# Performance work log

Hardware: AMD Instinct MI355X
Metric: run time of the kernel (lower is better)

## Reference

```python
import jax, jax.numpy as jnp
import numpy as np

N_NODES = 10000
N_EDGES = 160000
NEG_SLOPE = 0.2


def setup_inputs() -> dict:
    key = jax.random.key(0)
    ks = jax.random.split(key, 24)

    def rn(k, shape, scale):
        return (jax.random.normal(k, shape, dtype=jnp.float32) * scale)

    inp = {
        "x": rn(ks[0], (N_NODES, 128), 1.0),
        "edge_index": jax.random.randint(ks[1], (2, N_EDGES), 0, N_NODES, dtype=jnp.int32),
        "edge_attr": rn(ks[2], (N_EDGES, 8), 1.0),
        # GATConv 1: 128 -> 64 (heads=1)
        "W1": rn(ks[3], (128, 64), 0.09), "as1": rn(ks[4], (64,), 0.1), "ad1": rn(ks[5], (64,), 0.1), "b1": rn(ks[6], (64,), 0.01),
        # GATConv 2: 64 -> 256
        "W2": rn(ks[7], (64, 256), 0.125), "as2": rn(ks[8], (256,), 0.06), "ad2": rn(ks[9], (256,), 0.06), "b2": rn(ks[10], (256,), 0.01),
        # GATConv 3: 256 -> 1024
        "W3": rn(ks[11], (256, 1024), 0.0625), "as3": rn(ks[12], (1024,), 0.03), "ad3": rn(ks[13], (1024,), 0.03), "b3": rn(ks[14], (1024,), 0.01),
        # Dense head
        "lw1": rn(ks[15], (1024, 512), 0.03), "lb1": rn(ks[16], (512,), 0.01),
        "lw2": rn(ks[17], (512, 10), 0.04), "lb2": rn(ks[18], (10,), 0.01),
    }
    return inp


def gat_layer(x, src, dst, W, a_s, a_d, b, n):
    """PyG GATConv, heads=1, concat=True, add_self_loops handled by caller via src/dst."""
    h = x @ W                                   # [N, F_out]
    e = jax.nn.leaky_relu((h @ a_s)[src] + (h @ a_d)[dst], NEG_SLOPE)  # [E']
    m = jax.ops.segment_max(e, dst, num_segments=n)
    ex = jnp.exp(e - m[dst])
    denom = jax.ops.segment_sum(ex, dst, num_segments=n)
    alpha = ex / denom[dst]                     # scatter-softmax over incoming edges
    out = jax.ops.segment_sum(alpha[:, None] * h[src], dst, num_segments=n)
    return out + b


def reference(x, edge_index, edge_attr, W1, as1, ad1, b1, W2, as2, ad2, b2,
              W3, as3, ad3, b3, lw1, lb1, lw2, lb2):
    # edge_attr is accepted but ignored (GATConv built without edge_dim)
    n = x.shape[0]
    loops = jnp.arange(n, dtype=edge_index.dtype)  # add_self_loops=True
    src = jnp.concatenate([edge_index[0], loops])
    dst = jnp.concatenate([edge_index[1], loops])

    h = jax.nn.relu(gat_layer(x, src, dst, W1, as1, ad1, b1, n))
    h = jax.nn.relu(gat_layer(h, src, dst, W2, as2, ad2, b2, n))
    h = jax.nn.relu(gat_layer(h, src, dst, W3, as3, ad3, b3, n))

    pooled = jnp.max(h, axis=0, keepdims=True)  # global_max_pool, batch=None -> [1, 1024]
    z = jax.nn.relu(pooled @ lw1 + lb1)
    z = z @ lw2 + lb2
    return jax.nn.log_softmax(z, axis=1)
```

## Files before the change

kernel.cpp:

```cpp
#include <hip/hip_runtime.h>
#include <hip/hip_bf16.h>
#include <math.h>

#define NEG_SLOPE 0.2f
typedef unsigned short u16;
typedef short bf16x8 __attribute__((ext_vector_type(8)));
typedef float f32x4 __attribute__((ext_vector_type(4)));

__device__ __forceinline__ float bfu2f(u16 u) { return __uint_as_float(((unsigned)u) << 16); }
__device__ __forceinline__ u16 f2bu(float v) { return __bfloat16_as_ushort(__float2bfloat16(v)); }

__device__ __forceinline__ void gload_lds16(const void* g, void* l) {
    __builtin_amdgcn_global_load_lds((const __attribute__((address_space(1))) void*)g,
                                     (__attribute__((address_space(3))) void*)l, 16, 0, 0);
}

__global__ void prep_kernel(int* deg, int* cursor, float* pooled, int N,
                            const float* __restrict__ x, u16* __restrict__ xb,
                            const float* __restrict__ W1, u16* __restrict__ Wt1,
                            const float* __restrict__ W2, u16* __restrict__ Wt2,
                            const float* __restrict__ W3, u16* __restrict__ Wt3,
                            const float* __restrict__ as2, const float* __restrict__ ad2,
                            const float* __restrict__ as3, const float* __restrict__ ad3,
                            float* __restrict__ ws2, float* __restrict__ wd2,
                            float* __restrict__ ws3, float* __restrict__ wd3,
                            int c0, int c1, int c2, int c3, int c4) {
    int bid = blockIdx.x, tid = threadIdx.x;
    if (bid < c0) {
        int i = bid * 256 + tid;
        if (i < N) { deg[i] = 0; cursor[i] = 0; }
        if (i < 1024) pooled[i] = 0.f;
    } else if (bid < c1) {
        int i = (bid - c0) * 256 + tid;
        if (i < N * 128) xb[i] = f2bu(x[i]);
    } else if (bid < c2) {
        int i = (bid - c1) * 256 + tid;
        int k = i % 128, f = i / 128;
        Wt1[i] = f2bu(W1[k * 64 + f]);
    } else if (bid < c3) {
        int i = (bid - c2) * 256 + tid;
        int k = i % 64, f = i / 64;
        Wt2[i] = f2bu(W2[k * 256 + f]);
    } else if (bid < c4) {
        int i = (bid - c3) * 256 + tid;
        int k = i % 256, f = i / 256;
        Wt3[i] = f2bu(W3[(size_t)k * 1024 + f]);
    } else {
        int wv = ((bid - c4) * 256 + tid) >> 6;
        int lane = tid & 63;
        const float *W, *va, *vd; float *os, *od; int F, row;
        if (wv < 64) { W = W2; va = as2; vd = ad2; F = 256; row = wv; os = ws2; od = wd2; }
        else if (wv < 320) { W = W3; va = as3; vd = ad3; F = 1024; row = wv - 64; os = ws3; od = wd3; }
        else return;
        const float* wr = W + (size_t)row * F;
        float ss = 0.f, dd = 0.f;
        for (int f = lane; f < F; f += 64) { float wvv = wr[f]; ss += wvv * va[f]; dd += wvv * vd[f]; }
        for (int off = 32; off; off >>= 1) { ss += __shfl_xor(ss, off); dd += __shfl_xor(dd, off); }
        if (lane == 0) { os[row] = ss; od[row] = dd; }
    }
}

__global__ void count_kernel(const int* __restrict__ edst, int E, int N, int* deg) {
    int i = blockIdx.x * blockDim.x + threadIdx.x;
    int total = E + N;
    if (i >= total) return;
    int dn = (i < E) ? edst[i] : (i - E);
    atomicAdd(&deg[dn], 1);
}

__global__ void scan_kernel(const int* __restrict__ deg, int N, int* __restrict__ offsets) {
    __shared__ int part[257];
    int tid = threadIdx.x;
    int chunk = (N + 255) / 256;
    int begin = tid * chunk;
    int fin = begin + chunk; if (fin > N) fin = N; if (begin > N) begin = N;
    int sum = 0;
    for (int i = begin; i < fin; ++i) sum += deg[i];
    part[tid] = sum;
    __syncthreads();
    if (tid == 0) {
        int acc = 0;
        for (int t = 0; t < 256; ++t) { int v = part[t]; part[t] = acc; acc += v; }
        part[256] = acc;
    }
    __syncthreads();
    int acc = part[tid];
    for (int i = begin; i < fin; ++i) { offsets[i] = acc; acc += deg[i]; }
    if (tid == 255) offsets[N] = part[256];
}

__global__ void scatter_kernel(const int* __restrict__ esrc, const int* __restrict__ edst,
                               int E, int N, const int* __restrict__ offsets,
                               int* cursor, int* __restrict__ srcg) {
    int i = blockIdx.x * blockDim.x + threadIdx.x;
    int total = E + N;
    if (i >= total) return;
    int sn, dn;
    if (i < E) { sn = esrc[i]; dn = edst[i]; } else { sn = i - E; dn = i - E; }
    int pos = atomicAdd(&cursor[dn], 1);
    srcg[offsets[dn] + pos] = sn;
}

template <int K, int MR, bool BIASRELU, bool SD_EPI>
__global__ __launch_bounds__(256) void mfma_gemm(const u16* __restrict__ A,
                                                 const u16* __restrict__ Wt,
                                                 u16* __restrict__ C,
                                                 const float* __restrict__ bias,
                                                 int M, int F,
                                                 const float* __restrict__ asv,
                                                 const float* __restrict__ adv,
                                                 float* __restrict__ s_out,
                                                 float* __restrict__ d_out) {
    constexpr int NK = K / 32;
    int tid = threadIdx.x;
    int w = tid >> 6, l = tid & 63;
    int l15 = l & 15, q = l >> 4;
    int bm = blockIdx.x * (64 * MR);
    int bn = blockIdx.y * 64;
    int r0 = bm + w * (16 * MR);

    const u16* aptr[MR];
    int row[MR];
#pragma unroll
    for (int mr = 0; mr < MR; ++mr) {
        int r = r0 + mr * 16 + l15;
        row[mr] = r;
        int ar = (r < M) ? r : (M - 1);
        aptr[mr] = A + (size_t)ar * K + 8 * q;
    }
    const u16* bptr[4];
#pragma unroll
    for (int nt = 0; nt < 4; ++nt)
        bptr[nt] = Wt + (size_t)(bn + nt * 16 + l15) * K + 8 * q;

    f32x4 acc[MR][4];
#pragma unroll
    for (int mr = 0; mr < MR; ++mr)
#pragma unroll
        for (int nt = 0; nt < 4; ++nt) acc[mr][nt] = (f32x4){0.f, 0.f, 0.f, 0.f};

    bf16x8 a_cur[MR], b_cur[4], a_nxt[MR], b_nxt[4];
#pragma unroll
    for (int mr = 0; mr < MR; ++mr) a_cur[mr] = *(const bf16x8*)(aptr[mr]);
#pragma unroll
    for (int nt = 0; nt < 4; ++nt) b_cur[nt] = *(const bf16x8*)(bptr[nt]);

#pragma unroll
    for (int kk = 0; kk < NK; ++kk) {
        if (kk + 1 < NK) {
            int koff = (kk + 1) * 32;
#pragma unroll
            for (int mr = 0; mr < MR; ++mr) a_nxt[mr] = *(const bf16x8*)(aptr[mr] + koff);
#pragma unroll
            for (int nt = 0; nt < 4; ++nt) b_nxt[nt] = *(const bf16x8*)(bptr[nt] + koff);
        }
#pragma unroll
        for (int mr = 0; mr < MR; ++mr)
#pragma unroll
            for (int nt = 0; nt < 4; ++nt)
                acc[mr][nt] = __builtin_amdgcn_mfma_f32_16x16x32_bf16(b_cur[nt], a_cur[mr], acc[mr][nt], 0, 0, 0);
        if (kk + 1 < NK) {
#pragma unroll
            for (int mr = 0; mr < MR; ++mr) a_cur[mr] = a_nxt[mr];
#pragma unroll
            for (int nt = 0; nt < 4; ++nt) b_cur[nt] = b_nxt[nt];
        }
    }

#pragma unroll
    for (int mr = 0; mr < MR; ++mr) {
        if (row[mr] >= M) continue;
#pragma unroll
        for (int nt = 0; nt < 4; ++nt) {
            int col = bn + nt * 16 + 4 * q;
            ushort4 st;
#pragma unroll
            for (int r = 0; r < 4; ++r) {
                float v = acc[mr][nt][r];
                if (BIASRELU) { v += bias[col + r]; v = fmaxf(v, 0.f); }
                ((u16*)&st)[r] = f2bu(v);
            }
            *(ushort4*)(C + (size_t)row[mr] * F + col) = st;
        }
    }

    if constexpr (SD_EPI) {
        float ss = 0.f, dd = 0.f;
#pragma unroll
        for (int nt = 0; nt < 4; ++nt)
#pragma unroll
            for (int r = 0; r < 4; ++r) {
                int col = nt * 16 + 4 * q + r;
                float v = acc[0][nt][r];
                ss += v * asv[col];
                dd += v * adv[col];
            }
        ss += __shfl_xor(ss, 16); ss += __shfl_xor(ss, 32);
        dd += __shfl_xor(dd, 16); dd += __shfl_xor(dd, 32);
        if (q == 0 && row[0] < M) { s_out[row[0]] = ss; d_out[row[0]] = dd; }
    }
}

__global__ __launch_bounds__(512) void gemm3_kernel(const u16* __restrict__ A,
                                                    const u16* __restrict__ Wt,
                                                    const float* __restrict__ bias,
                                                    int M,
                                                    float* __restrict__ pmaxbuf) {
    constexpr int K = 256;
    constexpr int ABYTES = 128 * 512;
    __shared__ char lds[2 * ABYTES];
    int tid = threadIdx.x;
    int w = tid >> 6, lane = tid & 63;
    int w2 = w >> 2, wc = w & 3;
    int l15 = lane & 15, q = lane >> 4;
    int bid = blockIdx.x;
    int rb = bid >> 2, cbp = bid & 3;
    int bm = rb * 128;

#pragma unroll
    for (int it = 0; it < 8; ++it) {
        int c = it * 512 + tid;
        int row = c >> 5, kc = c & 31;
        int arow = bm + row; if (arow >= M) arow = M - 1;
        gload_lds16(A + (size_t)arow * K + ((kc ^ (row & 7)) * 8),
                    lds + (size_t)(it * 512 + (tid & ~63)) * 16);
    }

    const char* abase = lds;
    char* bldst = lds + ABYTES;

    for (int half = 0; half < 2; ++half) {
        if (half) __syncthreads();
        int bn = cbp * 256 + half * 128;
#pragma unroll
        for (int it = 0; it < 8; ++it) {
            int c = it * 512 + tid;
            int col = c >> 5, kc = c & 31;
            gload_lds16(Wt + (size_t)(bn + col) * K + ((kc ^ (col & 7)) * 8),
                        bldst + (size_t)(it * 512 + (tid & ~63)) * 16);
        }
        __syncthreads();

        f32x4 acc[4][2];
#pragma unroll
        for (int mr = 0; mr < 4; ++mr)
#pragma unroll
            for (int nt = 0; nt < 2; ++nt) acc[mr][nt] = (f32x4){0.f, 0.f, 0.f, 0.f};

        const char* bbase = bldst;
#pragma unroll
        for (int kk = 0; kk < 8; ++kk) {
            int c = kk * 4 + q;
            bf16x8 af[4], bfr[2];
#pragma unroll
            for (int mr = 0; mr < 4; ++mr) {
                int row = w2 * 64 + mr * 16 + l15;
                af[mr] = *(const bf16x8*)(abase + row * 512 + ((c ^ (row & 7)) * 16));
            }
#pragma unroll
            for (int nt = 0; nt < 2; ++nt) {
                int col = wc * 32 + nt * 16 + l15;
                bfr[nt] = *(const bf16x8*)(bbase + col * 512 + ((c ^ (col & 7)) * 16));
            }
#pragma unroll
            for (int mr = 0; mr < 4; ++mr)
#pragma unroll
                for (int nt = 0; nt < 2; ++nt)
                    acc[mr][nt] = __builtin_amdgcn_mfma_f32_16x16x32_bf16(bfr[nt], af[mr], acc[mr][nt], 0, 0, 0);
        }

        float pmax[2][4];
#pragma unroll
        for (int nt = 0; nt < 2; ++nt)
#pragma unroll
            for (int r = 0; r < 4; ++r) pmax[nt][r] = 0.f;
#pragma unroll
        for (int mr = 0; mr < 4; ++mr) {
            bool valid = (bm + w2 * 64 + mr * 16 + l15) < M;
#pragma unroll
            for (int nt = 0; nt < 2; ++nt)
#pragma unroll
                for (int r = 0; r < 4; ++r) {
                    float v = acc[mr][nt][r] + bias[bn + wc * 32 + nt * 16 + 4 * q + r];
                    v = fmaxf(v, 0.f);
                    if (valid) pmax[nt][r] = fmaxf(pmax[nt][r], v);
                }
        }
#pragma unroll
        for (int nt = 0; nt < 2; ++nt)
#pragma unroll
            for (int r = 0; r < 4; ++r) {
#pragma unroll
                for (int msk = 1; msk < 16; msk <<= 1)
                    pmax[nt][r] = fmaxf(pmax[nt][r], __shfl_xor(pmax[nt][r], msk));
            }
        if (l15 == 0) {
#pragma unroll
            for (int nt = 0; nt < 2; ++nt)
#pragma unroll
                for (int r = 0; r < 4; ++r)
                    pmaxbuf[(size_t)(rb * 2 + w2) * 1024 + bn + wc * 32 + nt * 16 + 4 * q + r] = pmax[nt][r];
        }
    }
}

__global__ void sd_kernel(const u16* __restrict__ h, const float* __restrict__ a_s,
                          const float* __restrict__ a_d, int N, int F,
                          float* __restrict__ s, float* __restrict__ d) {
    int wave = (blockIdx.x * blockDim.x + threadIdx.x) >> 6;
    int lane = threadIdx.x & 63;
    if (wave >= N) return;
    const u16* hrow = h + (size_t)wave * F;
    float ss = 0.f, dd = 0.f;
    for (int f = lane * 4; f < F; f += 256) {
        ushort4 u = *reinterpret_cast<const ushort4*>(hrow + f);
        float4 av = *reinterpret_cast<const float4*>(a_s + f);
        float4 dv = *reinterpret_cast<const float4*>(a_d + f);
        float h0 = bfu2f(u.x), h1 = bfu2f(u.y), h2 = bfu2f(u.z), h3 = bfu2f(u.w);
        ss += h0 * av.x + h1 * av.y + h2 * av.z + h3 * av.w;
        dd += h0 * dv.x + h1 * dv.y + h2 * dv.z + h3 * dv.w;
    }
    for (int off = 32; off; off >>= 1) { ss += __shfl_xor(ss, off); dd += __shfl_xor(dd, off); }
    if (lane == 0) { s[wave] = ss; d[wave] = dd; }
}

__global__ void alpha_kernel(const float* __restrict__ sv, const float* __restrict__ dvec,
                             const int* __restrict__ srcg, const int* __restrict__ offsets,
                             int N, float* __restrict__ ag) {
    int n = (blockIdx.x * blockDim.x + threadIdx.x) >> 6;
    int lane = threadIdx.x & 63;
    if (n >= N) return;
    int start = offsets[n], end = offsets[n + 1];
    float dval = dvec[n];
    if (end - start <= 64) {
        int j0 = start + lane;
        float e0 = -INFINITY;
        if (j0 < end) {
            float v = sv[srcg[j0]] + dval;
            e0 = (v >= 0.f) ? v : NEG_SLOPE * v;
        }
        float m = e0;
#pragma unroll
        for (int off = 32; off; off >>= 1) m = fmaxf(m, __shfl_xor(m, off));
        float p = (j0 < end) ? expf(e0 - m) : 0.f;
        float ls = p;
#pragma unroll
        for (int off = 32; off; off >>= 1) ls += __shfl_xor(ls, off);
        if (j0 < end) ag[j0] = p / ls;
    } else {
        float lmax = -INFINITY;
        for (int j = start + lane; j < end; j += 64) {
            float v = sv[srcg[j]] + dval; v = (v >= 0.f) ? v : NEG_SLOPE * v;
            lmax = fmaxf(lmax, v);
        }
#pragma unroll
        for (int off = 32; off; off >>= 1) lmax = fmaxf(lmax, __shfl_xor(lmax, off));
        float ls = 0.f;
        for (int j = start + lane; j < end; j += 64) {
            float v = sv[srcg[j]] + dval; v = (v >= 0.f) ? v : NEG_SLOPE * v;
            ls += expf(v - lmax);
        }
#pragma unroll
        for (int off = 32; off; off >>= 1) ls += __shfl_xor(ls, off);
        float inv = 1.f / ls;
        for (int j = start + lane; j < end; j += 64) {
            float v = sv[srcg[j]] + dval; v = (v >= 0.f) ? v : NEG_SLOPE * v;
            ag[j] = expf(v - lmax) * inv;
        }
    }
}

template <int F, int FS>
__global__ __launch_bounds__(256) void gather_kernel(const u16* __restrict__ h,
                                                     const float* __restrict__ ag,
                                                     const int* __restrict__ srcg,
                                                     const int* __restrict__ offsets,
                                                     u16* __restrict__ out) {
    constexpr int FB = F / FS;
    constexpr int VPT = FB / 64;
    __shared__ float aL[256];
    __shared__ int sL[256];
    __shared__ float red[3][FB];
    int n = blockIdx.x;
    int f0 = blockIdx.y * FB;
    int tid = threadIdx.x, w = tid >> 6, lane = tid & 63;
    int start = offsets[n], end = offsets[n + 1];
    int deg = end - start;
    float acc0 = 0.f, acc1 = 0.f;

    for (int base = 0; base < deg; base += 256) {
        int cnt = deg - base; if (cnt > 256) cnt = 256;
        if (base) __syncthreads();
        if (tid < cnt) { aL[tid] = ag[start + base + tid]; sL[tid] = srcg[start + base + tid]; }
        __syncthreads();
        int j = w;
        for (; j + 12 < cnt; j += 16) {
            float a0 = aL[j], a1 = aL[j + 4], a2 = aL[j + 8], a3 = aL[j + 12];
            const u16* p0 = h + (size_t)sL[j] * F + f0 + lane * VPT;
            const u16* p1 = h + (size_t)sL[j + 4] * F + f0 + lane * VPT;
            const u16* p2 = h + (size_t)sL[j + 8] * F + f0 + lane * VPT;
            const u16* p3 = h + (size_t)sL[j + 12] * F + f0 + lane * VPT;
            ushort2 u0 = *(const ushort2*)p0;
            ushort2 u1 = *(const ushort2*)p1;
            ushort2 u2 = *(const ushort2*)p2;
            ushort2 u3 = *(const ushort2*)p3;
            acc0 += a0 * bfu2f(u0.x) + a1 * bfu2f(u1.x) + a2 * bfu2f(u2.x) + a3 * bfu2f(u3.x);
            acc1 += a0 * bfu2f(u0.y) + a1 * bfu2f(u1.y) + a2 * bfu2f(u2.y) + a3 * bfu2f(u3.y);
        }
        for (; j < cnt; j += 4) {
            float a = aL[j];
            ushort2 u = *(const ushort2*)(h + (size_t)sL[j] * F + f0 + lane * VPT);
            acc0 += a * bfu2f(u.x);
            acc1 += a * bfu2f(u.y);
        }
    }

    if (w > 0) { red[w - 1][lane * 2] = acc0; red[w - 1][lane * 2 + 1] = acc1; }
    __syncthreads();
    if (w != 0) return;
    ushort2 st;
    float x0 = acc0 + red[0][lane * 2] + red[1][lane * 2] + red[2][lane * 2];
    float x1 = acc1 + red[0][lane * 2 + 1] + red[1][lane * 2 + 1] + red[2][lane * 2 + 1];
    st.x = f2bu(x0); st.y = f2bu(x1);
    *(ushort2*)(out + (size_t)n * F + f0 + lane * 2) = st;
}

template <int F, bool BIASRELU, bool SD_EPI>
__global__ __launch_bounds__(256) void agg_kernel(const u16* __restrict__ h,
                                                  const float* __restrict__ sv,
                                                  const float* __restrict__ dvec,
                                                  const int* __restrict__ srcg,
                                                  const int* __restrict__ offsets,
                                                  const float* __restrict__ bias,
                                                  u16* __restrict__ out,
                                                  const float* __restrict__ wsv,
                                                  const float* __restrict__ wdv,
                                                  float* __restrict__ s_out,
                                                  float* __restrict__ d_out) {
    constexpr int VPT = F / 64;
    __shared__ float pL[256];
    __shared__ int sL[256];
    __shared__ float red[3][F];
    int n = blockIdx.x;
    int tid = threadIdx.x;
    int w = tid >> 6, lane = tid & 63;
    int start = offsets[n], end = offsets[n + 1];
    int deg = end - start;
    float dval = dvec[n];
    float acc[VPT];
#pragma unroll
    for (int v = 0; v < VPT; ++v) acc[v] = 0.f;
    float inv;

    auto gpoint = [&](int sn) { return h + (size_t)sn * F + lane * VPT; };
    auto accum = [&](float pw, const u16* hp) {
        if constexpr (VPT == 1) {
            acc[0] += pw * bfu2f(*hp);
        } else {
            ushort2 u = *(const ushort2*)hp;
            acc[0] += pw * bfu2f(u.x); acc[1] += pw * bfu2f(u.y);
        }
    };

    if (deg <= 256) {
        float e = -INFINITY;
        if (tid < deg) {
            int sn = srcg[start + tid];
            sL[tid] = sn;
            float v = sv[sn] + dval;
            e = (v >= 0.f) ? v : NEG_SLOPE * v;
        }
        pL[tid] = e;
        __syncthreads();
        float m = fmaxf(fmaxf(pL[lane], pL[lane + 64]), fmaxf(pL[lane + 128], pL[lane + 192]));
#pragma unroll
        for (int off2 = 32; off2; off2 >>= 1) m = fmaxf(m, __shfl_xor(m, off2));
        __syncthreads();
        float p = (tid < deg) ? expf(e - m) : 0.f;
        pL[tid] = p;
        __syncthreads();
        float t4 = (pL[lane] + pL[lane + 64]) + (pL[lane + 128] + pL[lane + 192]);
#pragma unroll
        for (int off2 = 32; off2; off2 >>= 1) t4 += __shfl_xor(t4, off2);
        inv = 1.f / t4;
        int jj = w;
        for (; jj + 12 < deg; jj += 16) {
            float p0 = pL[jj], p1 = pL[jj + 4], p2 = pL[jj + 8], p3 = pL[jj + 12];
            const u16* h0 = gpoint(sL[jj]);
            const u16* h1 = gpoint(sL[jj + 4]);
            const u16* h2 = gpoint(sL[jj + 8]);
            const u16* h3 = gpoint(sL[jj + 12]);
            accum(p0, h0); accum(p1, h1); accum(p2, h2); accum(p3, h3);
        }
        for (; jj < deg; jj += 4) accum(pL[jj], gpoint(sL[jj]));
    } else {
        float lmax = -INFINITY;
        for (int j = start + lane; j < end; j += 64) {
            float v = sv[srcg[j]] + dval; v = (v >= 0.f) ? v : NEG_SLOPE * v;
            lmax = fmaxf(lmax, v);
        }
#pragma unroll
        for (int off2 = 32; off2; off2 >>= 1) lmax = fmaxf(lmax, __shfl_xor(lmax, off2));
        float ls = 0.f;
        for (int j = start + lane; j < end; j += 64) {
            float v = sv[srcg[j]] + dval; v = (v >= 0.f) ? v : NEG_SLOPE * v;
            ls += expf(v - lmax);
        }
#pragma unroll
        for (int off2 = 32; off2; off2 >>= 1) ls += __shfl_xor(ls, off2);
        inv = 1.f / ls;
        for (int j = start + w; j < end; j += 4) {
            int sn = srcg[j];
            float e2 = sv[sn] + dval; e2 = (e2 >= 0.f) ? e2 : NEG_SLOPE * e2;
            accum(expf(e2 - lmax), gpoint(sn));
        }
    }

    if (w > 0) {
#pragma unroll
        for (int v = 0; v < VPT; ++v) red[w - 1][lane * VPT + v] = acc[v];
    }
    __syncthreads();
    if (w != 0) return;
    float res0 = 0.f;
    if constexpr (VPT == 1) {
        float xv = (acc[0] + red[0][lane] + red[1][lane] + red[2][lane]) * inv;
        if (BIASRELU) { xv += bias[lane]; xv = fmaxf(xv, 0.f); }
        res0 = xv;
        out[(size_t)n * F + lane] = f2bu(xv);
    } else {
        ushort2 st;
#pragma unroll
        for (int v = 0; v < VPT; ++v) {
            float xv = (acc[v] + red[0][lane * 2 + v] + red[1][lane * 2 + v] + red[2][lane * 2 + v]) * inv;
            if (BIASRELU) { xv += bias[lane * 2 + v]; xv = fmaxf(xv, 0.f); }
            ((u16*)&st)[v] = f2bu(xv);
        }
        *(ushort2*)(out + (size_t)n * F + lane * 2) = st;
    }
    if constexpr (SD_EPI) {
        float ss = res0 * wsv[lane], dd = res0 * wdv[lane];
        for (int off2 = 32; off2; off2 >>= 1) { ss += __shfl_xor(ss, off2); dd += __shfl_xor(dd, off2); }
        if (lane == 0) { s_out[n] = ss; d_out[n] = dd; }
    }
}

__global__ void head1ap_kernel(const float* __restrict__ pmaxbuf, int nslices,
                               const float* __restrict__ lw1, float* __restrict__ part) {
    __shared__ float pk[64];
    int tid = threadIdx.x;
    int k0 = blockIdx.y * 64;
    if (tid < 64) {
        float m = 0.f;
#pragma unroll 4
        for (int s = 0; s < nslices; ++s) m = fmaxf(m, pmaxbuf[(size_t)s * 1024 + k0 + tid]);
        pk[tid] = m;
    }
    __syncthreads();
    int j = blockIdx.x * 128 + tid;
    float acc = 0.f;
#pragma unroll 8
    for (int kk = 0; kk < 64; ++kk) acc += pk[kk] * lw1[(size_t)(k0 + kk) * 512 + j];
    part[blockIdx.y * 512 + j] = acc;
}

__global__ void head1bc_kernel(const float* __restrict__ part, const float* __restrict__ lb1,
                               const float* __restrict__ lw2, const float* __restrict__ lb2,
                               float* __restrict__ out) {
    __shared__ float zs[512];
    __shared__ float z2s[10];
    int tid = threadIdx.x;
    if (tid < 512) {
        float acc = lb1[tid];
#pragma unroll
        for (int t = 0; t < 16; ++t) acc += part[t * 512 + tid];
        zs[tid] = fmaxf(acc, 0.f);
    }
    __syncthreads();
    int w = tid >> 6, lane = tid & 63;
    if (w < 10) {
        float acc = 0.f;
#pragma unroll
        for (int kc = 0; kc < 8; ++kc) {
            int k = kc * 64 + lane;
            acc += zs[k] * lw2[k * 10 + w];
        }
        for (int off = 32; off; off >>= 1) acc += __shfl_xor(acc, off);
        if (lane == 0) z2s[w] = acc + lb2[w];
    }
    __syncthreads();
    if (tid == 0) {
        float m = z2s[0];
        for (int j = 1; j < 10; ++j) m = fmaxf(m, z2s[j]);
        float ssum = 0.f;
        for (int j = 0; j < 10; ++j) ssum += expf(z2s[j] - m);
        float lse = m + logf(ssum);
        for (int j = 0; j < 10; ++j) out[j] = z2s[j] - lse;
    }
}

extern "C" void kernel_launch(void* const* d_in, const int* in_sizes, int n_in,
                              void* d_out, int out_size, void* d_ws, size_t ws_size,
                              hipStream_t stream) {
    const float* x   = (const float*)d_in[0];
    const int* ei    = (const int*)d_in[1];
    const float* W1  = (const float*)d_in[3];
    const float* as1 = (const float*)d_in[4];
    const float* ad1 = (const float*)d_in[5];
    const float* b1  = (const float*)d_in[6];
    const float* W2  = (const float*)d_in[7];
    const float* as2 = (const float*)d_in[8];
    const float* ad2 = (const float*)d_in[9];
    const float* b2  = (const float*)d_in[10];
    const float* W3  = (const float*)d_in[11];
    const float* as3 = (const float*)d_in[12];
    const float* ad3 = (const float*)d_in[13];
    const float* b3  = (const float*)d_in[14];
    const float* lw1 = (const float*)d_in[15];
    const float* lb1 = (const float*)d_in[16];
    const float* lw2 = (const float*)d_in[17];
    const float* lb2 = (const float*)d_in[18];
    float* out = (float*)d_out;

    const int N = in_sizes[0] / 128;
    const int E = in_sizes[1] / 2;
    const int total = E + N;
    const int* esrc = ei;
    const int* edst = ei + E;

    char* base = (char*)d_ws;
    size_t off = 0;
    auto alloc = [&](size_t bytes) { void* p = base + off; off = (off + bytes + 255) & ~(size_t)255; return p; };
    u16* xb    = (u16*)alloc((size_t)N * 128 * 2);
    u16* h1    = (u16*)alloc((size_t)N * 64 * 2);
    u16* a1    = (u16*)alloc((size_t)N * 64 * 2);
    u16* agg2b = (u16*)alloc((size_t)N * 64 * 2);
    u16* a2    = (u16*)alloc((size_t)N * 256 * 2);
    u16* agg3b = (u16*)alloc((size_t)N * 256 * 2);
    u16* Wt1   = (u16*)alloc(128 * 64 * 2);
    u16* Wt2   = (u16*)alloc(64 * 256 * 2);
    u16* Wt3   = (u16*)alloc(256 * 1024 * 2);
    float* ws2 = (float*)alloc(64 * 4);
    float* wd2 = (float*)alloc(64 * 4);
    float* ws3 = (float*)alloc(256 * 4);
    float* wd3 = (float*)alloc(256 * 4);
    float* sbuf = (float*)alloc((size_t)N * 4);
    float* dbuf = (float*)alloc((size_t)N * 4);
    float* ag   = (float*)alloc((size_t)total * 4);
    float* pooled = (float*)alloc(1024 * 4);
    float* hpart  = (float*)alloc(16 * 512 * 4);
    int* deg     = (int*)alloc((size_t)N * 4);
    int* cursor  = (int*)alloc((size_t)N * 4);
    int* offsets = (int*)alloc((size_t)(N + 1) * 4);
    int* srcg    = (int*)alloc((size_t)total * 4);
    int nrb128g = (N + 127) / 128;
    float* pmaxbuf = (float*)alloc((size_t)nrb128g * 2 * 1024 * 4);

    const int TPB = 256;
    int gE = (total + TPB - 1) / TPB;
    int gW = (N + 3) / 4;
    int gR64 = (N + 63) / 64;
    int gR128 = (N + 127) / 128;

    int c0 = (N + 255) / 256;
    int c1 = c0 + (N * 128 + 255) / 256;
    int c2 = c1 + (128 * 64) / 256;
    int c3 = c2 + (64 * 256) / 256;
    int c4 = c3 + (256 * 1024) / 256;
    int gP = c4 + 80;
    prep_kernel<<<gP, TPB, 0, stream>>>(deg, cursor, pooled, N, x, xb,
                                        W1, Wt1, W2, Wt2, W3, Wt3,
                                        as2, ad2, as3, ad3, ws2, wd2, ws3, wd3,
                                        c0, c1, c2, c3, c4);

    count_kernel<<<gE, TPB, 0, stream>>>(edst, E, N, deg);
    scan_kernel<<<1, TPB, 0, stream>>>(deg, N, offsets);
    scatter_kernel<<<gE, TPB, 0, stream>>>(esrc, edst, E, N, offsets, cursor, srcg);

    mfma_gemm<128, 1, false, true><<<dim3(gR64, 1), TPB, 0, stream>>>(
        xb, Wt1, h1, nullptr, N, 64, as1, ad1, sbuf, dbuf);
    agg_kernel<64, true, true><<<N, TPB, 0, stream>>>(
        h1, sbuf, dbuf, srcg, offsets, b1, a1, ws2, wd2, sbuf, dbuf);

    agg_kernel<64, false, false><<<N, TPB, 0, stream>>>(
        a1, sbuf, dbuf, srcg, offsets, nullptr, agg2b, nullptr, nullptr, nullptr, nullptr);
    mfma_gemm<64, 2, true, false><<<dim3(gR128, 4), TPB, 0, stream>>>(
        agg2b, Wt2, a2, b2, N, 256, nullptr, nullptr, nullptr, nullptr);

    sd_kernel<<<gW, TPB, 0, stream>>>(a2, ws3, wd3, N, 256, sbuf, dbuf);
    alpha_kernel<<<gW, TPB, 0, stream>>>(sbuf, dbuf, srcg, offsets, N, ag);
    gather_kernel<256, 2><<<dim3(N, 2), TPB, 0, stream>>>(a2, ag, srcg, offsets, agg3b);
    gemm3_kernel<<<nrb128g * 4, 512, 0, stream>>>(agg3b, Wt3, b3, N, pmaxbuf);

    head1ap_kernel<<<dim3(4, 16), 128, 0, stream>>>(pmaxbuf, nrb128g * 2, lw1, hpart);
    head1bc_kernel<<<1, 640, 0, stream>>>(hpart, lb1, lw2, lb2, out);
}
```

Measured before the change: 190.1 us.

## Fuse x bf16 conversion into layer-1 GEMM, tile weight transposes, unroll gathers

The separate fp32-to-bf16 conversion of x in the prep kernel is dropped. A new gemm1 kernel instead reads fp32 x directly, converts it in registers, and double-buffers its loads. Weight transposes now go through 64x64 LDS tiles so both reads and writes are coalesced, and the unused pooled buffer init is removed. The gather loops in the aggregation kernels are unrolled from 4 to 8 neighbours per iteration to keep more loads in flight, at some cost in register pressure.

Measured after the change: 199.0 us. +4.6%, slower.

```diff
diff --git a/kernel.cpp b/kernel.cpp
--- a/kernel.cpp
+++ b/kernel.cpp
@@ -15,8 +15,7 @@
                                      (__attribute__((address_space(3))) void*)l, 16, 0, 0);
 }
 
-__global__ void prep_kernel(int* deg, int* cursor, float* pooled, int N,
-                            const float* __restrict__ x, u16* __restrict__ xb,
+__global__ void prep_kernel(int* deg, int* cursor, int N,
                             const float* __restrict__ W1, u16* __restrict__ Wt1,
                             const float* __restrict__ W2, u16* __restrict__ Wt2,
                             const float* __restrict__ W3, u16* __restrict__ Wt3,
@@ -24,29 +23,32 @@
                             const float* __restrict__ as3, const float* __restrict__ ad3,
                             float* __restrict__ ws2, float* __restrict__ wd2,
                             float* __restrict__ ws3, float* __restrict__ wd3,
-                            int c0, int c1, int c2, int c3, int c4) {
+                            int c0) {
+    __shared__ u16 sm[64][66];
     int bid = blockIdx.x, tid = threadIdx.x;
     if (bid < c0) {
         int i = bid * 256 + tid;
         if (i < N) { deg[i] = 0; cursor[i] = 0; }
-        if (i < 1024) pooled[i] = 0.f;
-    } else if (bid < c1) {
-        int i = (bid - c0) * 256 + tid;
-        if (i < N * 128) xb[i] = f2bu(x[i]);
-    } else if (bid < c2) {
-        int i = (bid - c1) * 256 + tid;
-        int k = i % 128, f = i / 128;
-        Wt1[i] = f2bu(W1[k * 64 + f]);
-    } else if (bid < c3) {
-        int i = (bid - c2) * 256 + tid;
-        int k = i % 64, f = i / 64;
-        Wt2[i] = f2bu(W2[k * 256 + f]);
-    } else if (bid < c4) {
-        int i = (bid - c3) * 256 + tid;
-        int k = i % 256, f = i / 256;
-        Wt3[i] = f2bu(W3[(size_t)k * 1024 + f]);
+    } else if (bid < c0 + 70) {
+        int tb = bid - c0;
+        const float* W; u16* Wt; int K, F, kt, ft;
+        if (tb < 2)      { W = W1; Wt = Wt1; K = 128; F = 64;   kt = tb;          ft = 0; }
+        else if (tb < 6) { W = W2; Wt = Wt2; K = 64;  F = 256;  kt = 0;           ft = tb - 2; }
+        else             { W = W3; Wt = Wt3; K = 256; F = 1024; kt = (tb - 6) & 3; ft = (tb - 6) >> 2; }
+        int ty = tid >> 6, tx = tid & 63;
+#pragma unroll
+        for (int r = 0; r < 16; ++r) {
+            int kl = r * 4 + ty;
+            sm[kl][tx] = f2bu(W[(size_t)(kt * 64 + kl) * F + ft * 64 + tx]);
+        }
+        __syncthreads();
+#pragma unroll
+        for (int r = 0; r < 16; ++r) {
+            int fl = r * 4 + ty;
+            Wt[(size_t)(ft * 64 + fl) * K + kt * 64 + tx] = sm[tx][fl];
+        }
     } else {
-        int wv = ((bid - c4) * 256 + tid) >> 6;
+        int wv = ((bid - c0 - 70) * 256 + tid) >> 6;
         int lane = tid & 63;
         const float *W, *va, *vd; float *os, *od; int F, row;
         if (wv < 64) { W = W2; va = as2; vd = ad2; F = 256; row = wv; os = ws2; od = wd2; }
@@ -101,16 +103,92 @@
     srcg[offsets[dn] + pos] = sn;
 }
 
-template <int K, int MR, bool BIASRELU, bool SD_EPI>
+__global__ __launch_bounds__(256) void gemm1_kernel(const float* __restrict__ X,
+                                                    const u16* __restrict__ Wt,
+                                                    u16* __restrict__ C,
+                                                    int M,
+                                                    const float* __restrict__ asv,
+                                                    const float* __restrict__ adv,
+                                                    float* __restrict__ s_out,
+                                                    float* __restrict__ d_out) {
+    constexpr int K = 128, NK = 4;
+    int tid = threadIdx.x;
+    int w = tid >> 6, l = tid & 63;
+    int l15 = l & 15, q = l >> 4;
+    int bm = blockIdx.x * 64;
+    int row = bm + w * 16 + l15;
+    int arow = (row < M) ? row : (M - 1);
+    const float* aptr = X + (size_t)arow * K + 8 * q;
+    const u16* bptr[4];
+#pragma unroll
+    for (int nt = 0; nt < 4; ++nt)
+        bptr[nt] = Wt + (size_t)(nt * 16 + l15) * K + 8 * q;
+
+    f32x4 acc[4];
+#pragma unroll
+    for (int nt = 0; nt < 4; ++nt) acc[nt] = (f32x4){0.f, 0.f, 0.f, 0.f};
+
+    float4 a0_cur = *(const float4*)(aptr);
+    float4 a1_cur = *(const float4*)(aptr + 4);
+    bf16x8 b_cur[4], b_nxt[4];
+    float4 a0_nxt, a1_nxt;
+#pragma unroll
+    for (int nt = 0; nt < 4; ++nt) b_cur[nt] = *(const bf16x8*)(bptr[nt]);
+
+#pragma unroll
+    for (int kk = 0; kk < NK; ++kk) {
+        if (kk + 1 < NK) {
+            int koff = (kk + 1) * 32;
+            a0_nxt = *(const float4*)(aptr + koff);
+            a1_nxt = *(const float4*)(aptr + koff + 4);
+#pragma unroll
+            for (int nt = 0; nt < 4; ++nt) b_nxt[nt] = *(const bf16x8*)(bptr[nt] + koff);
+        }
+        bf16x8 a8;
+        u16* ap = (u16*)&a8;
+        ap[0] = f2bu(a0_cur.x); ap[1] = f2bu(a0_cur.y); ap[2] = f2bu(a0_cur.z); ap[3] = f2bu(a0_cur.w);
+        ap[4] = f2bu(a1_cur.x); ap[5] = f2bu(a1_cur.y); ap[6] = f2bu(a1_cur.z); ap[7] = f2bu(a1_cur.w);
+#pragma unroll
+        for (int nt = 0; nt < 4; ++nt)
+            acc[nt] = __builtin_amdgcn_mfma_f32_16x16x32_bf16(b_cur[nt], a8, acc[nt], 0, 0, 0);
+        if (kk + 1 < NK) {
+            a0_cur = a0_nxt; a1_cur = a1_nxt;
+#pragma unroll
+            for (int nt = 0; nt < 4; ++nt) b_cur[nt] = b_nxt[nt];
+        }
+    }
+
+    if (row < M) {
+#pragma unroll
+        for (int nt = 0; nt < 4; ++nt) {
+            int col = nt * 16 + 4 * q;
+            ushort4 st;
+#pragma unroll
+            for (int r = 0; r < 4; ++r) ((u16*)&st)[r] = f2bu(acc[nt][r]);
+            *(ushort4*)(C + (size_t)row * 64 + col) = st;
+        }
+    }
+    float ss = 0.f, dd = 0.f;
+#pragma unroll
+    for (int nt = 0; nt < 4; ++nt)
+#pragma unroll
+        for (int r = 0; r < 4; ++r) {
+            int col = nt * 16 + 4 * q + r;
+            float v = acc[nt][r];
+            ss += v * asv[col];
+            dd += v * adv[col];
+        }
+    ss += __shfl_xor(ss, 16); ss += __shfl_xor(ss, 32);
+    dd += __shfl_xor(dd, 16); dd += __shfl_xor(dd, 32);
+    if (q == 0 && row < M) { s_out[row] = ss; d_out[row] = dd; }
+}
+
+template <int K, int MR, bool BIASRELU>
 __global__ __launch_bounds__(256) void mfma_gemm(const u16* __restrict__ A,
                                                  const u16* __restrict__ Wt,
                                                  u16* __restrict__ C,
                                                  const float* __restrict__ bias,
-                                                 int M, int F,
-                                                 const float* __restrict__ asv,
-                                                 const float* __restrict__ adv,
-                                                 float* __restrict__ s_out,
-                                                 float* __restrict__ d_out) {
+                                                 int M, int F) {
     constexpr int NK = K / 32;
     int tid = threadIdx.x;
     int w = tid >> 6, l = tid & 63;
@@ -182,22 +260,6 @@
             }
             *(ushort4*)(C + (size_t)row[mr] * F + col) = st;
         }
-    }
-
-    if constexpr (SD_EPI) {
-        float ss = 0.f, dd = 0.f;
-#pragma unroll
-        for (int nt = 0; nt < 4; ++nt)
-#pragma unroll
-            for (int r = 0; r < 4; ++r) {
-                int col = nt * 16 + 4 * q + r;
-                float v = acc[0][nt][r];
-                ss += v * asv[col];
-                dd += v * adv[col];
-            }
-        ss += __shfl_xor(ss, 16); ss += __shfl_xor(ss, 32);
-        dd += __shfl_xor(dd, 16); dd += __shfl_xor(dd, 32);
-        if (q == 0 && row[0] < M) { s_out[row[0]] = ss; d_out[row[0]] = dd; }
     }
 }
 
@@ -394,18 +456,21 @@
         if (tid < cnt) { aL[tid] = ag[start + base + tid]; sL[tid] = srcg[start + base + tid]; }
         __syncthreads();
         int j = w;
-        for (; j + 12 < cnt; j += 16) {
-            float a0 = aL[j], a1 = aL[j + 4], a2 = aL[j + 8], a3 = aL[j + 12];
-            const u16* p0 = h + (size_t)sL[j] * F + f0 + lane * VPT;
-            const u16* p1 = h + (size_t)sL[j + 4] * F + f0 + lane * VPT;
-            const u16* p2 = h + (size_t)sL[j + 8] * F + f0 + lane * VPT;
-            const u16* p3 = h + (size_t)sL[j + 12] * F + f0 + lane * VPT;
-            ushort2 u0 = *(const ushort2*)p0;
-            ushort2 u1 = *(const ushort2*)p1;
-            ushort2 u2 = *(const ushort2*)p2;
-            ushort2 u3 = *(const ushort2*)p3;
-            acc0 += a0 * bfu2f(u0.x) + a1 * bfu2f(u1.x) + a2 * bfu2f(u2.x) + a3 * bfu2f(u3.x);
-            acc1 += a0 * bfu2f(u0.y) + a1 * bfu2f(u1.y) + a2 * bfu2f(u2.y) + a3 * bfu2f(u3.y);
+        for (; j + 28 < cnt; j += 32) {
+            float a0 = aL[j],      a1 = aL[j + 4],  a2 = aL[j + 8],  a3 = aL[j + 12];
+            float a4 = aL[j + 16], a5 = aL[j + 20], a6 = aL[j + 24], a7 = aL[j + 28];
+            ushort2 u0 = *(const ushort2*)(h + (size_t)sL[j] * F + f0 + lane * VPT);
+            ushort2 u1 = *(const ushort2*)(h + (size_t)sL[j + 4] * F + f0 + lane * VPT);
+            ushort2 u2 = *(const ushort2*)(h + (size_t)sL[j + 8] * F + f0 + lane * VPT);
+            ushort2 u3 = *(const ushort2*)(h + (size_t)sL[j + 12] * F + f0 + lane * VPT);
+            ushort2 u4 = *(const ushort2*)(h + (size_t)sL[j + 16] * F + f0 + lane * VPT);
+            ushort2 u5 = *(const ushort2*)(h + (size_t)sL[j + 20] * F + f0 + lane * VPT);
+            ushort2 u6 = *(const ushort2*)(h + (size_t)sL[j + 24] * F + f0 + lane * VPT);
+            ushort2 u7 = *(const ushort2*)(h + (size_t)sL[j + 28] * F + f0 + lane * VPT);
+            acc0 += a0 * bfu2f(u0.x) + a1 * bfu2f(u1.x) + a2 * bfu2f(u2.x) + a3 * bfu2f(u3.x)
+                  + a4 * bfu2f(u4.x) + a5 * bfu2f(u5.x) + a6 * bfu2f(u6.x) + a7 * bfu2f(u7.x);
+            acc1 += a0 * bfu2f(u0.y) + a1 * bfu2f(u1.y) + a2 * bfu2f(u2.y) + a3 * bfu2f(u3.y)
+                  + a4 * bfu2f(u4.y) + a5 * bfu2f(u5.y) + a6 * bfu2f(u6.y) + a7 * bfu2f(u7.y);
         }
         for (; j < cnt; j += 4) {
             float a = aL[j];
@@ -484,13 +549,15 @@
         for (int off2 = 32; off2; off2 >>= 1) t4 += __shfl_xor(t4, off2);
         inv = 1.f / t4;
         int jj = w;
-        for (; jj + 12 < deg; jj += 16) {
-            float p0 = pL[jj], p1 = pL[jj + 4], p2 = pL[jj + 8], p3 = pL[jj + 12];
-            const u16* h0 = gpoint(sL[jj]);
-            const u16* h1 = gpoint(sL[jj + 4]);
-            const u16* h2 = gpoint(sL[jj + 8]);
-            const u16* h3 = gpoint(sL[jj + 12]);
-            accum(p0, h0); accum(p1, h1); accum(p2, h2); accum(p3, h3);
+        for (; jj + 28 < deg; jj += 32) {
+            accum(pL[jj], gpoint(sL[jj]));
+            accum(pL[jj + 4], gpoint(sL[jj + 4]));
+            accum(pL[jj + 8], gpoint(sL[jj + 8]));
+            accum(pL[jj + 12], gpoint(sL[jj + 12]));
+            accum(pL[jj + 16], gpoint(sL[jj + 16]));
+            accum(pL[jj + 20], gpoint(sL[jj + 20]));
+            accum(pL[jj + 24], gpoint(sL[jj + 24]));
+            accum(pL[jj + 28], gpoint(sL[jj + 28]));
         }
         for (; jj < deg; jj += 4) accum(pL[jj], gpoint(sL[jj]));
     } else {
@@ -631,7 +698,6 @@
     char* base = (char*)d_ws;
     size_t off = 0;
     auto alloc = [&](size_t bytes) { void* p = base + off; off = (off + bytes + 255) & ~(size_t)255; return p; };
-    u16* xb    = (u16*)alloc((size_t)N * 128 * 2);
     u16* h1    = (u16*)alloc((size_t)N * 64 * 2);
     u16* a1    = (u16*)alloc((size_t)N * 64 * 2);
     u16* agg2b = (u16*)alloc((size_t)N * 64 * 2);
@@ -647,7 +713,6 @@
     float* sbuf = (float*)alloc((size_t)N * 4);
     float* dbuf = (float*)alloc((size_t)N * 4);
     float* ag   = (float*)alloc((size_t)total * 4);
-    float* pooled = (float*)alloc(1024 * 4);
     float* hpart  = (float*)alloc(16 * 512 * 4);
     int* deg     = (int*)alloc((size_t)N * 4);
     int* cursor  = (int*)alloc((size_t)N * 4);
@@ -663,29 +728,23 @@
     int gR128 = (N + 127) / 128;
 
     int c0 = (N + 255) / 256;
-    int c1 = c0 + (N * 128 + 255) / 256;
-    int c2 = c1 + (128 * 64) / 256;
-    int c3 = c2 + (64 * 256) / 256;
-    int c4 = c3 + (256 * 1024) / 256;
-    int gP = c4 + 80;
-    prep_kernel<<<gP, TPB, 0, stream>>>(deg, cursor, pooled, N, x, xb,
+    int gP = c0 + 70 + 80;
+    prep_kernel<<<gP, TPB, 0, stream>>>(deg, cursor, N,
                                         W1, Wt1, W2, Wt2, W3, Wt3,
-                                        as2, ad2, as3, ad3, ws2, wd2, ws3, wd3,
-                                        c0, c1, c2, c3, c4);
+                                        as2, ad2, as3, ad3, ws2, wd2, ws3, wd3, c0);
 
     count_kernel<<<gE, TPB, 0, stream>>>(edst, E, N, deg);
     scan_kernel<<<1, TPB, 0, stream>>>(deg, N, offsets);
     scatter_kernel<<<gE, TPB, 0, stream>>>(esrc, edst, E, N, offsets, cursor, srcg);
 
-    mfma_gemm<128, 1, false, true><<<dim3(gR64, 1), TPB, 0, stream>>>(
-        xb, Wt1, h1, nullptr, N, 64, as1, ad1, sbuf, dbuf);
+    gemm1_kernel<<<gR64, TPB, 0, stream>>>(x, Wt1, h1, N, as1, ad1, sbuf, dbuf);
     agg_kernel<64, true, true><<<N, TPB, 0, stream>>>(
         h1, sbuf, dbuf, srcg, offsets, b1, a1, ws2, wd2, sbuf, dbuf);
 
     agg_kernel<64, false, false><<<N, TPB, 0, stream>>>(
         a1, sbuf, dbuf, srcg, offsets, nullptr, agg2b, nullptr, nullptr, nullptr, nullptr);
-    mfma_gemm<64, 2, true, false><<<dim3(gR128, 4), TPB, 0, stream>>>(
-        agg2b, Wt2, a2, b2, N, 256, nullptr, nullptr, nullptr, nullptr);
+    mfma_gemm<64, 2, true><<<dim3(gR128, 4), TPB, 0, stream>>>(
+        agg2b, Wt2, a2, b2, N, 256);
 
     sd_kernel<<<gW, TPB, 0, stream>>>(a2, ws3, wd3, N, 256, sbuf, dbuf);
     alpha_kernel<<<gW, TPB, 0, stream>>>(sbuf, dbuf, srcg, offsets, N, ag);
```
